# Kernel tuning notes

Hardware: AMD Instinct MI355X
Metric: run time of the kernel (lower is better)

The kernel has to match this reference:

```python
import jax, jax.numpy as jnp
import numpy as np

N_NODES = 100000
N_EDGES = 3200000
N_GRAPHS = 4096
N_REL = 5
N_BASES = 4
HID = 32


def setup_inputs() -> dict:
    key = jax.random.key(0)
    ks = jax.random.split(key, 32)
    inp = {}
    inp['x'] = jax.random.normal(ks[0], (N_NODES, 4), dtype=jnp.float32)
    inp['edge_index'] = jax.random.randint(ks[1], (2, N_EDGES), 0, N_NODES, dtype=jnp.int64)
    inp['edge_type'] = jax.random.randint(ks[2], (N_EDGES,), 0, N_REL, dtype=jnp.int64)
    inp['user_idx'] = jax.random.randint(ks[3], (N_GRAPHS,), 0, N_NODES, dtype=jnp.int64)
    inp['item_idx'] = jax.random.randint(ks[4], (N_GRAPHS,), 0, N_NODES, dtype=jnp.int64)
    k = 5
    for l in range(4):
        in_c = 4 if l == 0 else HID
        inp[f'basis{l}'] = jax.random.normal(ks[k], (N_BASES, in_c, HID), dtype=jnp.float32) * 0.1; k += 1
        inp[f'comp{l}'] = jax.random.normal(ks[k], (N_REL, N_BASES), dtype=jnp.float32) * 0.5; k += 1
        inp[f'root{l}'] = jax.random.normal(ks[k], (in_c, HID), dtype=jnp.float32) * 0.1; k += 1
        inp[f'bias{l}'] = jax.random.normal(ks[k], (HID,), dtype=jnp.float32) * 0.01; k += 1
    inp['w1'] = jax.random.normal(ks[k], (256, 128), dtype=jnp.float32) * 0.05; k += 1
    inp['b1'] = jnp.zeros((128,), dtype=jnp.float32)
    inp['w2'] = jax.random.normal(ks[k], (128, 1), dtype=jnp.float32) * 0.05; k += 1
    inp['b2'] = jnp.zeros((1,), dtype=jnp.float32)
    return inp


def _rgcn_layer(x, src, key5, inv_cnt, basis, comp, root, bias, n_nodes):
    # mean-aggregate raw source features per (dst, relation): [N, R, in]
    agg = jax.ops.segment_sum(x[src], key5, num_segments=n_nodes * N_REL)
    agg = agg.reshape(n_nodes, N_REL, -1) * inv_cnt
    # basis-decomposed relation weights: W_r = sum_b comp[r,b] * basis[b]
    w = jnp.einsum('rb,bio->rio', comp, basis)  # [R, in, out]
    return jnp.einsum('nri,rio->no', agg, w) + x @ root + bias


def reference(x, edge_index, edge_type, user_idx, item_idx,
              basis0, comp0, root0, bias0,
              basis1, comp1, root1, bias1,
              basis2, comp2, root2, bias2,
              basis3, comp3, root3, bias3,
              w1, b1, w2, b2):
    n_nodes = x.shape[0]
    src, dst = edge_index[0], edge_index[1]
    key5 = dst * N_REL + edge_type  # combined (dst, relation) segment id
    cnt = jax.ops.segment_sum(jnp.ones_like(edge_type, dtype=x.dtype), key5,
                              num_segments=n_nodes * N_REL)
    inv_cnt = (1.0 / jnp.maximum(cnt, 1.0)).reshape(n_nodes, N_REL, 1)
    params = [(basis0, comp0, root0, bias0), (basis1, comp1, root1, bias1),
              (basis2, comp2, root2, bias2), (basis3, comp3, root3, bias3)]
    out = x
    hs = []
    for (basis, comp, root, bias) in params:
        out = jnp.tanh(_rgcn_layer(out, src, key5, inv_cnt, basis, comp, root, bias, n_nodes))
        hs.append(out)
    h = jnp.concatenate(hs, axis=1)            # [N, 128]
    g = jnp.concatenate([h[user_idx], h[item_idx]], axis=1)  # [B, 256]
    z = jax.nn.relu(g @ w1 + b1)
    return (z @ w2 + b2)[:, 0]
```

## Files before the change

kernel.cpp:

```cpp
#include <hip/hip_runtime.h>
#include <hip/hip_bf16.h>
#include <hip/hip_fp16.h>

#define N_NODES 100000
#define N_EDGES 3200000
#define N_GRAPHS 4096
#define N_REL 5
#define N_BASES 4
#define HID 32
#define SEG (N_NODES*N_REL)
#define DUMMY N_NODES

#define NBUCK 392
#define BCAP  10240
#define PBCAP 15360
#define NKEY  1280

typedef _Float16 half8 __attribute__((ext_vector_type(8)));
typedef float floatx4 __attribute__((ext_vector_type(4)));

static __global__ __launch_bounds__(256) void k_part(const int* __restrict__ ei,
                                                     const int* __restrict__ et,
                                                     int* __restrict__ gcur,
                                                     unsigned long long* __restrict__ part) {
    __shared__ int hcnt[NBUCK];
    __shared__ int lbase[NBUCK];
    int t = threadIdx.x;
    for (int k = t; k < NBUCK; k += 256) hcnt[k] = 0;
    __syncthreads();
    int e0 = blockIdx.x * 4096;
    int src[16], bkt[16], lkey[16];
#pragma unroll
    for (int j = 0; j < 16; j++) {
        int e = e0 + j * 256 + t;
        if (e < N_EDGES) {
            int s = ei[e];
            int d = ei[N_EDGES + e];
            int r = et[e];
            src[j] = s; bkt[j] = d >> 8; lkey[j] = ((d & 255) * 5) + r;
            atomicAdd(&hcnt[bkt[j]], 1);
        } else bkt[j] = -1;
    }
    __syncthreads();
    for (int k = t; k < NBUCK; k += 256) lbase[k] = atomicAdd(&gcur[k], hcnt[k]);
    __syncthreads();
    for (int k = t; k < NBUCK; k += 256) hcnt[k] = 0;
    __syncthreads();
#pragma unroll
    for (int j = 0; j < 16; j++) {
        if (bkt[j] >= 0) {
            int rank = atomicAdd(&hcnt[bkt[j]], 1);
            int p = lbase[bkt[j]] + rank;
            if (p < BCAP)
                part[(size_t)bkt[j] * BCAP + p] =
                    ((unsigned long long)(unsigned)lkey[j] << 32) | (unsigned)src[j];
        }
    }
}

static __global__ __launch_bounds__(512) void k_bsort(const unsigned long long* __restrict__ part,
                                                      const int* __restrict__ gcur,
                                                      int* __restrict__ offs,
                                                      int* __restrict__ cnt,
                                                      int* __restrict__ srcs) {
    __shared__ int lhist[NKEY];
    __shared__ int lscan[NKEY];
    __shared__ int sscan[256];
    __shared__ int lsrc[PBCAP];
    int b = blockIdx.x;
    int t = threadIdx.x;
    int n = gcur[b]; if (n > BCAP) n = BCAP;
    const unsigned long long* reg = part + (size_t)b * BCAP;

    for (int k = t; k < NKEY; k += 512) lhist[k] = 0;
    __syncthreads();
    for (int i = t; i < n; i += 512)
        atomicAdd(&lhist[(int)(reg[i] >> 32)], 1);
    __syncthreads();

    int loc[5]; int s5 = 0;
    if (t < 256) {
#pragma unroll
        for (int j = 0; j < 5; j++) { loc[j] = s5; s5 += (lhist[t * 5 + j] + 7) & ~7; }
        sscan[t] = s5;
    }
    __syncthreads();
    for (int off = 1; off < 256; off <<= 1) {
        int x = (t >= off && t < 256) ? sscan[t - off] : 0;
        __syncthreads();
        if (t < 256) sscan[t] += x;
        __syncthreads();
    }
    if (t < 256) {
        int excl = sscan[t] - s5;
#pragma unroll
        for (int j = 0; j < 5; j++) lscan[t * 5 + j] = excl + loc[j];
    }
    __syncthreads();

    int base = b * PBCAP;
    if (t < 256) {
#pragma unroll
        for (int j = 0; j < 5; j++) {
            int k = t * 5 + j;
            int segid = b * NKEY + k;
            if (segid < SEG) {
                cnt[segid]  = lhist[k];
                offs[segid] = base + lscan[k];
            }
        }
    }
    __syncthreads();
    for (int k = t; k < NKEY; k += 512) lhist[k] = 0;
    for (int i = t; i < PBCAP; i += 512) lsrc[i] = DUMMY;
    __syncthreads();
    for (int i = t; i < n; i += 512) {
        unsigned long long u = reg[i];
        int k = (int)(u >> 32);
        int pos = lscan[k] + atomicAdd(&lhist[k], 1);
        if (pos < PBCAP) lsrc[pos] = (int)(u & 0xffffffffULL);
    }
    __syncthreads();
    for (int i = t; i < PBCAP; i += 512) srcs[base + i] = lsrc[i];
}

static __global__ __launch_bounds__(256) void k_pad(const float* __restrict__ x,
                                                    __half* __restrict__ ht0,
                                                    __half* __restrict__ ht1,
                                                    __half* __restrict__ ht2,
                                                    __half* __restrict__ ht3,
                                                    __half* __restrict__ ht4,
                                                    int* __restrict__ srcs) {
    int tid = blockIdx.x * 256 + threadIdx.x;
    if (tid < (N_NODES + 1) * 32) {
        int nd = tid >> 5, ii = tid & 31;
        float v = (nd < N_NODES && ii < 4) ? x[(nd << 2) + ii] : 0.f;
        ht0[tid] = __float2half(v);
    } else {
        int r = tid - (N_NODES + 1) * 32;
        if (r < 128) {
            __half* hp = (r < 32) ? ht1 : (r < 64) ? ht2 : (r < 96) ? ht3 : ht4;
            hp[N_NODES * 32 + (r & 31)] = __float2half(0.f);
        } else if (r < 144) srcs[NBUCK * PBCAP + (r - 128)] = DUMMY;
    }
}

static __global__ __launch_bounds__(256) void k_wprepB(
    const float* __restrict__ ba0, const float* __restrict__ ro0,
    const float* __restrict__ ba1, const float* __restrict__ ro1,
    const float* __restrict__ ba2, const float* __restrict__ ro2,
    const float* __restrict__ ba3, const float* __restrict__ ro3,
    __half* __restrict__ Wb) {
    int idx = blockIdx.x * 256 + threadIdx.x;
    int j    = idx & 7;
    int lane = (idx >> 3) & 63;
    int tile = (idx >> 9) & 1;
    int ls   = idx >> 10;
    int l    = ls / 5;
    int s    = ls - l * 5;
    const float* basis = (l == 0) ? ba0 : (l == 1) ? ba1 : (l == 2) ? ba2 : ba3;
    const float* root  = (l == 0) ? ro0 : (l == 1) ? ro1 : (l == 2) ? ro2 : ro3;
    int in_c = (l == 0) ? 4 : HID;
    int k = s * 32 + ((lane >> 4) << 3) + j;
    int o = tile * 16 + (lane & 15);
    float v;
    if (k < 128) {
        int b = k >> 5, ii = k & 31;
        v = (ii < in_c) ? basis[(b * in_c + ii) * HID + o] : 0.f;
    } else {
        int ii = k - 128;
        v = (ii < in_c) ? root[ii * HID + o] : 0.f;
    }
    Wb[idx] = __float2half(v);
}

static __global__ __launch_bounds__(256) void k_wprepM(const float* __restrict__ w1,
                                                       __half* __restrict__ Wm) {
    int idx = blockIdx.x * 256 + threadIdx.x;
    int j    = idx & 7;
    int lane = (idx >> 3) & 63;
    int s    = (idx >> 9) & 7;
    int tile = idx >> 12;
    int k = s * 32 + ((lane >> 4) << 3) + j;
    int o = tile * 16 + (lane & 15);
    Wm[idx] = __float2half(w1[k * 128 + o]);
}

static __global__ __launch_bounds__(256, 8) void k_layer(
    const __half2* __restrict__ tab, const int* __restrict__ offs,
    const int* __restrict__ cnt, const int* __restrict__ srcs,
    const float* __restrict__ comp, const __half* __restrict__ Wbl,
    const float* __restrict__ bias, __half* __restrict__ hout) {
    __shared__ __align__(16) __half sAgg16[16 * 176];
    int t = threadIdx.x;
    int wave = t >> 6, q = (t >> 4) & 3, p = t & 15;

    float4 cw0 = *(const float4*)(comp + 0);
    float4 cw1 = *(const float4*)(comp + 4);
    float4 cw2 = *(const float4*)(comp + 8);
    float4 cw3 = *(const float4*)(comp + 12);
    float4 cw4 = *(const float4*)(comp + 16);

    int n = blockIdx.x * 16 + wave * 4 + q;
    int s5 = n * N_REL;
    int oo[6], cc[5];
#pragma unroll
    for (int r = 0; r < 5; r++) { oo[r] = offs[s5 + r]; cc[r] = cnt[s5 + r]; }
    oo[5] = oo[4] + ((cc[4] + 7) & ~7);

    __half2 selfh = tab[n * 16 + p];
    float a0x = 0.f, a0y = 0.f, a1x = 0.f, a1y = 0.f;
    float a2x = 0.f, a2y = 0.f, a3x = 0.f, a3y = 0.f;

#pragma unroll
    for (int r = 0; r < 5; r++) {
        int pR = oo[r], pr = oo[r + 1] - pR;
        const int* sp = srcs + pR;
        int4 e0 = *(const int4*)(sp);
        int4 e1 = *(const int4*)(sp + 4);
        __half2 g0 = tab[e0.x * 16 + p], g1 = tab[e0.y * 16 + p];
        __half2 g2 = tab[e0.z * 16 + p], g3 = tab[e0.w * 16 + p];
        __half2 g4 = tab[e1.x * 16 + p], g5 = tab[e1.y * 16 + p];
        __half2 g6 = tab[e1.z * 16 + p], g7 = tab[e1.w * 16 + p];
        __half2 sb = __hadd2(__hadd2(__hadd2(g0, g1), __hadd2(g2, g3)),
                             __hadd2(__hadd2(g4, g5), __hadd2(g6, g7)));
        float2 bf = __half22float2(sb);
        float Sx = bf.x, Sy = bf.y;
        for (int s8 = 8; s8 < pr; s8 += 8) {
            int4 f0 = *(const int4*)(sp + s8);
            int4 f1 = *(const int4*)(sp + s8 + 4);
            __half2 h0 = tab[f0.x * 16 + p], h1 = tab[f0.y * 16 + p];
            __half2 h2 = tab[f0.z * 16 + p], h3 = tab[f0.w * 16 + p];
            __half2 h4 = tab[f1.x * 16 + p], h5 = tab[f1.y * 16 + p];
            __half2 h6 = tab[f1.z * 16 + p], h7 = tab[f1.w * 16 + p];
            __half2 rb = __hadd2(__hadd2(__hadd2(h0, h1), __hadd2(h2, h3)),
                                 __hadd2(__hadd2(h4, h5), __hadd2(h6, h7)));
            float2 rf = __half22float2(rb);
            Sx += rf.x; Sy += rf.y;
        }
        int cr = cc[r];
        float ic = (cr > 0) ? __builtin_amdgcn_rcpf((float)cr) : 0.f;
        float scx = Sx * ic, scy = Sy * ic;
        float4 cw = (r == 0) ? cw0 : (r == 1) ? cw1 : (r == 2) ? cw2
                  : (r == 3) ? cw3 : cw4;
        a0x += cw.x * scx; a0y += cw.x * scy;
        a1x += cw.y * scx; a1y += cw.y * scy;
        a2x += cw.z * scx; a2y += cw.z * scy;
        a3x += cw.w * scx; a3y += cw.w * scy;
    }
    int nl = wave * 4 + q;
    __half2* row = (__half2*)(sAgg16 + nl * 176);
    row[p]      = __float22half2_rn(make_float2(a0x, a0y));
    row[16 + p] = __float22half2_rn(make_float2(a1x, a1y));
    row[32 + p] = __float22half2_rn(make_float2(a2x, a2y));
    row[48 + p] = __float22half2_rn(make_float2(a3x, a3y));
    row[64 + p] = selfh;
    __syncthreads();

    if (wave < 2) {
        int lane = t & 63;
        floatx4 acc = {0.f, 0.f, 0.f, 0.f};
        const __half* aBase = sAgg16 + (lane & 15) * 176 + ((lane >> 4) << 3);
        const __half* bBase = Wbl + wave * 512 + lane * 8;
#pragma unroll
        for (int s = 0; s < 5; s++) {
            half8 a = *(const half8*)(aBase + s * 32);
            half8 b = *(const half8*)(bBase + s * 1024);
            acc = __builtin_amdgcn_mfma_f32_16x16x32_f16(a, b, acc, 0, 0, 0);
        }
        int o = wave * 16 + (lane & 15);
        float bi = bias[o];
#pragma unroll
        for (int r = 0; r < 4; r++) {
            int node = blockIdx.x * 16 + ((lane >> 4) << 2) + r;
            hout[node * 32 + o] = __float2half(tanhf(acc[r] + bi));
        }
    }
}

static __global__ __launch_bounds__(256) void k_mlp(
    const __half* __restrict__ h1, const __half* __restrict__ h2,
    const __half* __restrict__ h3, const __half* __restrict__ h4,
    const int* __restrict__ uidx, const int* __restrict__ iidx,
    const __half* __restrict__ Wm, const float* __restrict__ b1,
    const float* __restrict__ w2, const float* __restrict__ b2,
    float* __restrict__ out) {
    __shared__ __align__(16) __half sg[16 * 264];
    __shared__ float sacc[4][16];
    int t = threadIdx.x, wave = t >> 6, lane = t & 63;
    int g0 = blockIdx.x * 16;
    int lt = lane >> 4, lp = lane & 15;
    const __half* htab = (lt == 0) ? h1 : (lt == 1) ? h2 : (lt == 2) ? h3 : h4;
#pragma unroll
    for (int gg2 = 0; gg2 < 4; gg2++) {
        int gg = wave * 4 + gg2;
        int g = g0 + gg;
        int u = uidx[g], it = iidx[g];
        __half2* dst = (__half2*)(sg + gg * 264);
        dst[lt * 16 + lp]      = ((const __half2*)(htab + u * 32))[lp];
        dst[64 + lt * 16 + lp] = ((const __half2*)(htab + it * 32))[lp];
    }
    __syncthreads();
    floatx4 acc0 = {0.f, 0.f, 0.f, 0.f}, acc1 = {0.f, 0.f, 0.f, 0.f};
    const __half* aBase = sg + (lane & 15) * 264 + ((lane >> 4) << 3);
    const __half* bB0 = Wm + (wave * 2 + 0) * 4096 + lane * 8;
    const __half* bB1 = Wm + (wave * 2 + 1) * 4096 + lane * 8;
#pragma unroll
    for (int s = 0; s < 8; s++) {
        half8 a  = *(const half8*)(aBase + s * 32);
        half8 f0 = *(const half8*)(bB0 + s * 512);
        half8 f1 = *(const half8*)(bB1 + s * 512);
        acc0 = __builtin_amdgcn_mfma_f32_16x16x32_f16(a, f0, acc0, 0, 0, 0);
        acc1 = __builtin_amdgcn_mfma_f32_16x16x32_f16(a, f1, acc1, 0, 0, 0);
    }
    int o0 = wave * 32 + (lane & 15);
    int o1 = o0 + 16;
    float b10 = b1[o0], b11 = b1[o1], w20 = w2[o0], w21 = w2[o1];
#pragma unroll
    for (int r = 0; r < 4; r++) {
        float z0 = fmaxf(acc0[r] + b10, 0.f);
        float z1 = fmaxf(acc1[r] + b11, 0.f);
        float v = z0 * w20 + z1 * w21;
#pragma unroll
        for (int off = 1; off < 16; off <<= 1) v += __shfl_xor(v, off);
        if ((lane & 15) == 0) sacc[wave][((lane >> 4) << 2) + r] = v;
    }
    __syncthreads();
    if (t < 16)
        out[g0 + t] = sacc[0][t] + sacc[1][t] + sacc[2][t] + sacc[3][t] + b2[0];
}

extern "C" void kernel_launch(void* const* d_in, const int* in_sizes, int n_in,
                              void* d_out, int out_size, void* d_ws, size_t ws_size,
                              hipStream_t stream) {
    const float* x  = (const float*)d_in[0];
    const int*   ei = (const int*)d_in[1];
    const int*   et = (const int*)d_in[2];
    const int*   ui = (const int*)d_in[3];
    const int*   ii = (const int*)d_in[4];
    const float* w1 = (const float*)d_in[21];
    const float* b1 = (const float*)d_in[22];
    const float* w2 = (const float*)d_in[23];
    const float* b2 = (const float*)d_in[24];

    char* ws = (char*)d_ws;
    if (ws_size < 92167680UL) return;
    int*    gcur = (int*)(ws + 0);
    int*    offs = (int*)(ws + 2048);
    int*    cnt  = (int*)(ws + 2002176);
    int*    srcs = (int*)(ws + 4002304);
    __half* Wb   = (__half*)(ws + 28086912);
    __half* Wm   = (__half*)(ws + 28127872);
    __half* ht0  = (__half*)(ws + 28193536);
    __half* ht1  = (__half*)(ws + 34593664);
    __half* ht2  = (__half*)(ws + 40993792);
    __half* ht3  = (__half*)(ws + 47393920);
    __half* ht4  = (__half*)(ws + 53794048);
    unsigned long long* part = (unsigned long long*)(ws + 34593664);

    hipMemsetAsync(gcur, 0, NBUCK * 4, stream);

    k_part<<<782, 256, 0, stream>>>(ei, et, gcur, part);
    k_bsort<<<NBUCK, 512, 0, stream>>>(part, gcur, offs, cnt, srcs);
    k_pad<<<12501, 256, 0, stream>>>(x, ht0, ht1, ht2, ht3, ht4, srcs);
    k_wprepB<<<80, 256, 0, stream>>>(
        (const float*)d_in[5],  (const float*)d_in[7],
        (const float*)d_in[9],  (const float*)d_in[11],
        (const float*)d_in[13], (const float*)d_in[15],
        (const float*)d_in[17], (const float*)d_in[19], Wb);
    k_wprepM<<<128, 256, 0, stream>>>(w1, Wm);

    __half* tabs[5] = {ht0, ht1, ht2, ht3, ht4};
    for (int l = 0; l < 4; l++) {
        const float* comp = (const float*)d_in[6 + 4 * l];
        const float* bias = (const float*)d_in[8 + 4 * l];
        k_layer<<<6250, 256, 0, stream>>>((const __half2*)tabs[l], offs, cnt,
                                          srcs, comp, Wb + l * 5120, bias,
                                          tabs[l + 1]);
    }
    k_mlp<<<256, 256, 0, stream>>>(ht1, ht2, ht3, ht4, ui, ii, Wm, b1, w2, b2,
                                   (float*)d_out);
}
```

Baseline: 368.2 us.

## Stage partitioned edges in shared memory for coalesced bucket writes

The edge partition kernel now builds a per-tile histogram and exclusive scan, scatters the packed edges into a shared-memory staging buffer ordered by bucket, then writes them to global memory in contiguous runs per bucket. This replaces scattered 8-byte global writes with mostly coalesced ones. The tile is doubled to 8192 edges, which halves the global atomic traffic. In exchange the destination index is read twice, there is an extra scan pass with several block barriers, and 64KB of LDS per block limits occupancy.

```diff
diff --git a/kernel.cpp b/kernel.cpp
--- a/kernel.cpp
+++ b/kernel.cpp
@@ -15,6 +15,7 @@
 #define BCAP  10240
 #define PBCAP 15360
 #define NKEY  1280
+#define PTILE 8192
 
 typedef _Float16 half8 __attribute__((ext_vector_type(8)));
 typedef float floatx4 __attribute__((ext_vector_type(4)));
@@ -23,38 +24,62 @@
                                                      const int* __restrict__ et,
                                                      int* __restrict__ gcur,
                                                      unsigned long long* __restrict__ part) {
-    __shared__ int hcnt[NBUCK];
+    __shared__ unsigned long long stage[PTILE];
+    __shared__ int hist[NBUCK];
+    __shared__ int lofs[NBUCK];
     __shared__ int lbase[NBUCK];
+    __shared__ int sscan[256];
     int t = threadIdx.x;
-    for (int k = t; k < NBUCK; k += 256) hcnt[k] = 0;
-    __syncthreads();
-    int e0 = blockIdx.x * 4096;
-    int src[16], bkt[16], lkey[16];
-#pragma unroll
-    for (int j = 0; j < 16; j++) {
+    int e0 = blockIdx.x * PTILE;
+    int tile_n = N_EDGES - e0; if (tile_n > PTILE) tile_n = PTILE;
+
+    for (int k = t; k < NBUCK; k += 256) hist[k] = 0;
+    __syncthreads();
+    for (int j = 0; j < PTILE / 256; j++) {
+        int e = e0 + j * 256 + t;
+        if (e < N_EDGES) atomicAdd(&hist[ei[N_EDGES + e] >> 8], 1);
+    }
+    __syncthreads();
+    int h0 = (2 * t     < NBUCK) ? hist[2 * t]     : 0;
+    int h1 = (2 * t + 1 < NBUCK) ? hist[2 * t + 1] : 0;
+    int s2 = h0 + h1;
+    sscan[t] = s2;
+    __syncthreads();
+    for (int off = 1; off < 256; off <<= 1) {
+        int xv = (t >= off) ? sscan[t - off] : 0;
+        __syncthreads();
+        sscan[t] += xv;
+        __syncthreads();
+    }
+    int excl = sscan[t] - s2;
+    if (2 * t     < NBUCK) lofs[2 * t]     = excl;
+    if (2 * t + 1 < NBUCK) lofs[2 * t + 1] = excl + h0;
+    for (int k = t; k < NBUCK; k += 256) lbase[k] = atomicAdd(&gcur[k], hist[k]);
+    __syncthreads();
+    for (int k = t; k < NBUCK; k += 256) hist[k] = 0;
+    __syncthreads();
+    for (int j = 0; j < PTILE / 256; j++) {
         int e = e0 + j * 256 + t;
         if (e < N_EDGES) {
             int s = ei[e];
             int d = ei[N_EDGES + e];
             int r = et[e];
-            src[j] = s; bkt[j] = d >> 8; lkey[j] = ((d & 255) * 5) + r;
-            atomicAdd(&hcnt[bkt[j]], 1);
-        } else bkt[j] = -1;
-    }
-    __syncthreads();
-    for (int k = t; k < NBUCK; k += 256) lbase[k] = atomicAdd(&gcur[k], hcnt[k]);
-    __syncthreads();
-    for (int k = t; k < NBUCK; k += 256) hcnt[k] = 0;
-    __syncthreads();
-#pragma unroll
-    for (int j = 0; j < 16; j++) {
-        if (bkt[j] >= 0) {
-            int rank = atomicAdd(&hcnt[bkt[j]], 1);
-            int p = lbase[bkt[j]] + rank;
-            if (p < BCAP)
-                part[(size_t)bkt[j] * BCAP + p] =
-                    ((unsigned long long)(unsigned)lkey[j] << 32) | (unsigned)src[j];
+            int bkt = d >> 8;
+            int lkey = ((d & 255) * 5) + r;
+            int rank = atomicAdd(&hist[bkt], 1);
+            stage[lofs[bkt] + rank] =
+                ((unsigned long long)(unsigned)((bkt << 16) | lkey) << 32) | (unsigned)s;
         }
+    }
+    __syncthreads();
+    for (int i = t; i < tile_n; i += 256) {
+        unsigned long long u = stage[i];
+        unsigned hi = (unsigned)(u >> 32);
+        int bkt = hi >> 16;
+        unsigned long long lkey = hi & 0xFFFFu;
+        int pos = lbase[bkt] + (i - lofs[bkt]);
+        if (pos < BCAP)
+            part[(size_t)bkt * BCAP + pos] = (lkey << 32) | (u & 0xffffffffULL);
     }
 }
 
@@ -360,7 +385,7 @@
 
     hipMemsetAsync(gcur, 0, NBUCK * 4, stream);
 
-    k_part<<<782, 256, 0, stream>>>(ei, et, gcur, part);
+    k_part<<<(N_EDGES + PTILE - 1) / PTILE, 256, 0, stream>>>(ei, et, gcur, part);
     k_bsort<<<NBUCK, 512, 0, stream>>>(part, gcur, offs, cnt, srcs);
     k_pad<<<12501, 256, 0, stream>>>(x, ht0, ht1, ht2, ht3, ht4, srcs);
     k_wprepB<<<80, 256, 0, stream>>>(
```

Measured after the change: 353.5 us. 1.04x faster.
